# Optimization experiments

Hardware: AMD Instinct MI355X
Metric: run time of the kernel (lower is better)

The kernel has to match this reference:

```python
import jax, jax.numpy as jnp
import numpy as np
from jax import lax

B_, H_, W_ = 2, 32, 32
D_MODEL, D_STATE, D_CONV, DT_RANK, K = 192, 16, 3, 12, 4
D_INNER = 2 * D_MODEL


def setup_inputs() -> dict:
    key = jax.random.key(0)
    ks = jax.random.split(key, 10)
    x = jax.random.normal(ks[0], (B_, H_, W_, D_MODEL), jnp.float32)
    x_cross = jax.random.normal(ks[1], (B_, H_, W_, D_MODEL), jnp.float32)
    in_proj_w = jax.random.normal(ks[2], (2 * D_INNER, D_MODEL), jnp.float32) * 0.02
    in_proj_cross_w = jax.random.normal(ks[3], (D_INNER, D_MODEL), jnp.float32) * 0.02
    conv_w = jax.random.normal(ks[4], (D_INNER, 1, D_CONV, D_CONV), jnp.float32) * 0.1  # depthwise
    conv_b = jnp.zeros((D_INNER,), jnp.float32)
    x_proj_weight = jax.random.normal(ks[5], (K, DT_RANK + 2 * D_STATE, D_INNER), jnp.float32) * 0.02
    dt_std = DT_RANK ** -0.5
    dt_projs_weight = jax.random.uniform(ks[6], (K, D_INNER, DT_RANK), jnp.float32, -dt_std, dt_std)
    # inverse-softplus init of dt bias, as in CSS2D.dt_init
    dt = jnp.exp(jax.random.uniform(ks[7], (K, D_INNER), jnp.float32)
                 * (np.log(0.1) - np.log(0.001)) + np.log(0.001))
    dt = jnp.clip(dt, 1e-4, None)
    dt_projs_bias = dt + jnp.log(-jnp.expm1(-dt))
    A_logs = jnp.log(jnp.tile(jnp.arange(1, D_STATE + 1, dtype=jnp.float32)[None, :], (K * D_INNER, 1)))
    Ds = jnp.ones((K * D_INNER,), jnp.float32)
    out_norm_g = jnp.ones((D_INNER,), jnp.float32)
    out_norm_b = jnp.zeros((D_INNER,), jnp.float32)
    out_proj_w = jax.random.normal(ks[8], (D_MODEL, D_INNER), jnp.float32) * 0.02
    return dict(x=x, x_cross=x_cross, in_proj_w=in_proj_w, in_proj_cross_w=in_proj_cross_w,
                conv_w=conv_w, conv_b=conv_b, x_proj_weight=x_proj_weight,
                dt_projs_weight=dt_projs_weight, dt_projs_bias=dt_projs_bias,
                A_logs=A_logs, Ds=Ds, out_norm_g=out_norm_g, out_norm_b=out_norm_b,
                out_proj_w=out_proj_w)


def _css2d_forward(x, x_cross, in_proj_w, in_proj_cross_w, conv_w, conv_b,
                   x_proj_weight, dt_projs_weight, dt_projs_bias, A_logs, Ds,
                   out_norm_g, out_norm_b, out_proj_w):
    B, H, W, _ = x.shape
    L = H * W
    Din, N, R = D_INNER, D_STATE, DT_RANK

    # in projections
    xz = x @ in_proj_w.T                       # [B,H,W,2*Din]
    xp, z = jnp.split(xz, 2, axis=-1)
    xc = x_cross @ in_proj_cross_w.T           # [B,H,W,Din]

    # depthwise conv + SiLU on main branch (NCHW)
    xh = jnp.transpose(xp, (0, 3, 1, 2))
    pad = (D_CONV - 1) // 2
    xh = lax.conv_general_dilated(xh, conv_w, (1, 1), [(pad, pad), (pad, pad)],
                                  dimension_numbers=('NCHW', 'OIHW', 'NCHW'),
                                  feature_group_count=Din)
    xh = jax.nn.silu(xh + conv_b[None, :, None, None])
    xc = jnp.transpose(xc, (0, 3, 1, 2))       # [B,Din,H,W]

    def cross_scan(t):  # [B,Din,H,W] -> [B,4,Din,L]
        a = t.reshape(B, Din, L)
        b = jnp.transpose(t, (0, 1, 3, 2)).reshape(B, Din, L)
        s = jnp.stack([a, b], axis=1)
        return jnp.concatenate([s, jnp.flip(s, axis=-1)], axis=1)

    xs = cross_scan(xh)
    xsc = cross_scan(xc)

    # dt/B/C projections from the cross stream
    x_dbl = jnp.einsum('bkdl,kcd->bkcl', xsc, x_proj_weight)
    dts, Bmat, Cmat = jnp.split(x_dbl, [R, R + N], axis=2)  # [B,K,R,L],[B,K,N,L],[B,K,N,L]
    dts = jnp.einsum('bkrl,kdr->bkdl', dts, dt_projs_weight)

    A = -jnp.exp(A_logs).reshape(K, Din, N)
    delta = jax.nn.softplus(dts + dt_projs_bias[None, :, :, None])  # [B,K,Din,L]

    # selective scan: h_{t} = exp(delta*A)*h_{t-1} + delta*B_t*u_t ; y_t = C_t . h_t
    dA = jnp.exp(jnp.einsum('bkdl,kdn->lbkdn', delta, A))   # [L,B,K,Din,N]
    dBu = jnp.einsum('bkdl,bknl->lbkdn', delta * xs, Bmat)  # [L,B,K,Din,N]
    Ct = jnp.transpose(Cmat, (3, 0, 1, 2))                  # [L,B,K,N]

    def step(h, inp):
        dA_t, dBu_t, c = inp
        h = dA_t * h + dBu_t
        return h, jnp.einsum('bkdn,bkn->bkd', h, c)

    h0 = jnp.zeros((B, K, Din, N), x.dtype)
    _, ys = lax.scan(step, h0, (dA, dBu, Ct))               # ys: [L,B,K,Din]
    out_y = jnp.transpose(ys, (1, 2, 3, 0)) + xs * Ds.reshape(1, K, Din, 1)  # [B,K,Din,L]

    # merge the 4 directions
    inv_y = jnp.flip(out_y[:, 2:4], axis=-1)
    wh = lambda t: jnp.transpose(t.reshape(B, Din, W, H), (0, 1, 3, 2)).reshape(B, Din, L)
    y = out_y[:, 0] + inv_y[:, 0] + wh(out_y[:, 1]) + wh(inv_y[:, 1])
    y = jnp.transpose(y, (0, 2, 1)).reshape(B, H, W, Din)

    # LayerNorm(out_norm)
    mu = jnp.mean(y, axis=-1, keepdims=True)
    var = jnp.mean((y - mu) ** 2, axis=-1, keepdims=True)
    y = (y - mu) * lax.rsqrt(var + 1e-5) * out_norm_g + out_norm_b

    y = y * jax.nn.silu(z)
    return y @ out_proj_w.T


def reference(x, x_cross, in_proj_w, in_proj_cross_w, conv_w, conv_b, x_proj_weight,
              dt_projs_weight, dt_projs_bias, A_logs, Ds, out_norm_g, out_norm_b, out_proj_w):
    return _css2d_forward(x, x_cross, in_proj_w, in_proj_cross_w, conv_w, conv_b,
                          x_proj_weight, dt_projs_weight, dt_projs_bias, A_logs, Ds,
                          out_norm_g, out_norm_b, out_proj_w)
```

## Files before the change

### kernel.cpp

```cpp
#include <hip/hip_runtime.h>
#include <hip/hip_bf16.h>
#include <math.h>

#define BB 2
#define HH 32
#define WW 32
#define LL 1024
#define DM 192
#define DI 384
#define NS 16
#define RR 12
#define KK 4
#define CC 44
#define NC 64
#define LC 16
#define NCH 3072
#define GB 49152

__device__ __forceinline__ int bfflag(const void* dsv){
  return ((const unsigned*)dsv)[0] != 0x3F800000u;
}
__device__ __forceinline__ float ldin(const void* p, int i, int bf) {
  if (bf) {
    unsigned v = ((const unsigned short*)p)[i];
    return __uint_as_float(v << 16);
  }
  return ((const float*)p)[i];
}
__device__ __forceinline__ float4 ldin4(const void* p, int i, int bf) {
  if (bf) {
    ushort4 u = ((const ushort4*)p)[i >> 2];
    float4 r;
    r.x = __uint_as_float((unsigned)u.x << 16);
    r.y = __uint_as_float((unsigned)u.y << 16);
    r.z = __uint_as_float((unsigned)u.z << 16);
    r.w = __uint_as_float((unsigned)u.w << 16);
    return r;
  }
  return ((const float4*)p)[i >> 2];
}
__device__ __forceinline__ float sigm(float x){ return 1.f/(1.f + __expf(-x)); }
__device__ __forceinline__ float softplusf(float x){ return (x > 20.f) ? x : log1pf(__expf(x)); }

__device__ __forceinline__ int permk(int k, int l){
  if (k == 0) return l;
  if (k == 2) return LL-1-l;
  int lr = (k == 3) ? (LL-1-l) : l;
  return (lr & 31)*WW + (lr >> 5);
}

__global__ __launch_bounds__(256) void k_inproj(const void* x, const void* xcr,
    const void* wi, const void* wc, const void* dsv,
    float* __restrict__ xp, float* __restrict__ z, float* __restrict__ xcd){
  const int bf = bfflag(dsv);
  __shared__ float As[64][65];
  __shared__ float Ws[64][65];
  const int mb = blockIdx.x & 31;
  const int nb = blockIdx.x >> 5;
  const int pos0 = mb*64;
  const int row0g = nb*64;
  const void* src  = (row0g < 768) ? x  : xcr;
  const void* wsrc = (row0g < 768) ? wi : wc;
  const int wrow0 = (row0g < 768) ? row0g : row0g - 768;
  const int t = threadIdx.x;
  const int tx = t & 15, ty = t >> 4;
  float acc[4][4];
  #pragma unroll
  for (int m=0;m<4;m++){
    #pragma unroll
    for (int n=0;n<4;n++) acc[m][n]=0.f;
  }
  for (int k0 = 0; k0 < DM; k0 += 64){
    for (int i = t*4; i < 4096; i += 1024){
      const int p = i >> 6, kk = i & 63;
      const float4 va = ldin4(src,  (pos0 +p)*DM + k0 + kk, bf);
      As[kk+0][p]=va.x; As[kk+1][p]=va.y; As[kk+2][p]=va.z; As[kk+3][p]=va.w;
      const float4 vw = ldin4(wsrc, (wrow0+p)*DM + k0 + kk, bf);
      Ws[kk+0][p]=vw.x; Ws[kk+1][p]=vw.y; Ws[kk+2][p]=vw.z; Ws[kk+3][p]=vw.w;
    }
    __syncthreads();
    #pragma unroll 8
    for (int kk = 0; kk < 64; kk++){
      const float4 a4 = *(const float4*)&As[kk][ty*4];
      const float4 w4 = *(const float4*)&Ws[kk][tx*4];
      acc[0][0]=fmaf(a4.x,w4.x,acc[0][0]); acc[0][1]=fmaf(a4.x,w4.y,acc[0][1]);
      acc[0][2]=fmaf(a4.x,w4.z,acc[0][2]); acc[0][3]=fmaf(a4.x,w4.w,acc[0][3]);
      acc[1][0]=fmaf(a4.y,w4.x,acc[1][0]); acc[1][1]=fmaf(a4.y,w4.y,acc[1][1]);
      acc[1][2]=fmaf(a4.y,w4.z,acc[1][2]); acc[1][3]=fmaf(a4.y,w4.w,acc[1][3]);
      acc[2][0]=fmaf(a4.z,w4.x,acc[2][0]); acc[2][1]=fmaf(a4.z,w4.y,acc[2][1]);
      acc[2][2]=fmaf(a4.z,w4.z,acc[2][2]); acc[2][3]=fmaf(a4.z,w4.w,acc[2][3]);
      acc[3][0]=fmaf(a4.w,w4.x,acc[3][0]); acc[3][1]=fmaf(a4.w,w4.y,acc[3][1]);
      acc[3][2]=fmaf(a4.w,w4.z,acc[3][2]); acc[3][3]=fmaf(a4.w,w4.w,acc[3][3]);
    }
    __syncthreads();
  }
  float* dst; int obase;
  if (row0g < 384)      { dst = xp;  obase = row0g; }
  else if (row0g < 768) { dst = z;   obase = row0g-384; }
  else                  { dst = xcd; obase = row0g-768; }
  #pragma unroll
  for (int m=0;m<4;m++){
    const int pos = pos0 + ty*4 + m;
    *(float4*)&dst[(size_t)pos*DI + obase + tx*4] =
        make_float4(acc[m][0], acc[m][1], acc[m][2], acc[m][3]);
  }
}

__global__ __launch_bounds__(256) void k_conv(const float* __restrict__ xp,
    const void* cw, const void* cb, const void* dsv, float* __restrict__ xh){
  const int bf = bfflag(dsv);
  const int idx = blockIdx.x*256 + threadIdx.x;
  const int d = idx % DI;
  const int l = (idx / DI) % LL;
  const int b = idx / (DI*LL);
  const int h = l >> 5, w = l & 31;
  float acc = ldin(cb, d, bf);
  #pragma unroll
  for (int kh=0; kh<3; kh++){
    const int hh = h + kh - 1;
    if (hh < 0 || hh >= HH) continue;
    #pragma unroll
    for (int kw=0; kw<3; kw++){
      const int ww2 = w + kw - 1;
      if (ww2 < 0 || ww2 >= WW) continue;
      acc = fmaf(xp[(b*LL + hh*WW + ww2)*DI + d], ldin(cw, d*9 + kh*3 + kw, bf), acc);
    }
  }
  xh[idx] = acc * sigm(acc);
}

__global__ __launch_bounds__(384) void k_xscanA(const float* __restrict__ xc,
    const float* __restrict__ xh, const void* xpw, const void* dtw,
    const void* dtb, const void* alogs, const void* dsv,
    float* __restrict__ delta, float* __restrict__ Bm, float* __restrict__ Cm,
    float* __restrict__ Acum, float* __restrict__ Hend){
  const int bf = bfflag(dsv);
  const int blk = blockIdx.x;
  const int b = blk >> 8;
  const int k = (blk >> 6) & 3;
  const int c = blk & 63;
  const int l0 = c * LC;
  const int t = threadIdx.x;
  __shared__ float xrow[LC][DI+4];
  __shared__ float dtsS[LC][RR];
  __shared__ float Bs[LC][NS];
  for (int idx = t; idx < LC*96; idx += 384){
    const int j = idx / 96, cc = idx % 96;
    const int pl = permk(k, l0 + j);
    *(float4*)&xrow[j][cc*4] = *(const float4*)&xc[(b*LL + pl)*DI + cc*4];
  }
  __syncthreads();
  for (int idx = t; idx < CC*LC; idx += 384){
    const int ch = idx >> 4, j = idx & 15;
    const int wbase = (k*CC + ch)*DI;
    float a0=0.f, a1=0.f, a2=0.f, a3=0.f;
    for (int cc = 0; cc < 96; cc += 4){
      const float4 w0 = ldin4(xpw, wbase + (cc+0)*4, bf);
      const float4 w1 = ldin4(xpw, wbase + (cc+1)*4, bf);
      const float4 w2 = ldin4(xpw, wbase + (cc+2)*4, bf);
      const float4 w3 = ldin4(xpw, wbase + (cc+3)*4, bf);
      const float4 x0 = *(const float4*)&xrow[j][(cc+0)*4];
      const float4 x1 = *(const float4*)&xrow[j][(cc+1)*4];
      const float4 x2 = *(const float4*)&xrow[j][(cc+2)*4];
      const float4 x3 = *(const float4*)&xrow[j][(cc+3)*4];
      a0 = fmaf(w0.x,x0.x, fmaf(w0.y,x0.y, fmaf(w0.z,x0.z, fmaf(w0.w,x0.w, a0))));
      a1 = fmaf(w1.x,x1.x, fmaf(w1.y,x1.y, fmaf(w1.z,x1.z, fmaf(w1.w,x1.w, a1))));
      a2 = fmaf(w2.x,x2.x, fmaf(w2.y,x2.y, fmaf(w2.z,x2.z, fmaf(w2.w,x2.w, a2))));
      a3 = fmaf(w3.x,x3.x, fmaf(w3.y,x3.y, fmaf(w3.z,x3.z, fmaf(w3.w,x3.w, a3))));
    }
    const float acc = (a0+a1)+(a2+a3);
    if (ch < RR)          dtsS[j][ch] = acc;
    else if (ch < RR+NS){ Bs[j][ch-RR] = acc;
                          Bm[((b*KK+k)*LL + l0+j)*NS + (ch-RR)]    = acc; }
    else                  Cm[((b*KK+k)*LL + l0+j)*NS + (ch-RR-NS)] = acc;
  }
  __syncthreads();
  {
    const int d = t;
    float w[RR];
    #pragma unroll
    for (int q = 0; q < 3; q++){
      const float4 w4 = ldin4(dtw, (k*DI+d)*RR + q*4, bf);
      w[q*4+0]=w4.x; w[q*4+1]=w4.y; w[q*4+2]=w4.z; w[q*4+3]=w4.w;
    }
    const float bias = ldin(dtb, k*DI + d, bf);
    #pragma unroll
    for (int j = 0; j < LC; j++){
      float acc = bias;
      #pragma unroll
      for (int r = 0; r < RR; r++) acc = fmaf(w[r], dtsS[j][r], acc);
      xrow[j][d] = softplusf(acc);
    }
  }
  __syncthreads();
  for (int idx = t; idx < LC*96; idx += 384){
    const int j = idx / 96, cc = idx % 96;
    *(float4*)&delta[((b*KK+k)*LL + l0+j)*DI + cc*4] = *(const float4*)&xrow[j][cc*4];
  }
  {
    const int d = t;
    float An[NS];
    #pragma unroll
    for (int q = 0; q < 4; q++){
      const float4 a4 = ldin4(alogs, (k*DI + d)*NS + q*4, bf);
      An[q*4+0] = -__expf(a4.x); An[q*4+1] = -__expf(a4.y);
      An[q*4+2] = -__expf(a4.z); An[q*4+3] = -__expf(a4.w);
    }
    float h[NS], Ac[NS];
    #pragma unroll
    for (int n = 0; n < NS; n++){ h[n] = 0.f; Ac[n] = 1.f; }
    const int xbase = b*LL*DI + d;
    #pragma unroll 4
    for (int j = 0; j < LC; j++){
      const int l = l0 + j;
      const float dl = xrow[j][d];
      const float u  = xh[xbase + permk(k,l)*DI];
      const float dlu = dl*u;
      #pragma unroll
      for (int n = 0; n < NS; n++){
        const float e = __expf(dl*An[n]);
        Ac[n] *= e;
        h[n] = fmaf(e, h[n], dlu*Bs[j][n]);
      }
    }
    const int chain = (b*KK + k)*DI + d;
    const int obase = (c*NCH + chain)*NS;
    #pragma unroll
    for (int q = 0; q < 4; q++){
      *(float4*)&Acum[obase + q*4] = make_float4(Ac[q*4],Ac[q*4+1],Ac[q*4+2],Ac[q*4+3]);
      *(float4*)&Hend[obase + q*4] = make_float4(h[q*4],h[q*4+1],h[q*4+2],h[q*4+3]);
    }
  }
}

__global__ __launch_bounds__(256) void k_scanB(const float* __restrict__ Acum,
    float* __restrict__ Hend){
  const int g = blockIdx.x*256 + threadIdx.x;
  float h = 0.f;
  #pragma unroll 8
  for (int c = 0; c < NC; c++){
    const float a = Acum[c*GB + g];
    const float e = Hend[c*GB + g];
    Hend[c*GB + g] = h;
    h = fmaf(a, h, e);
  }
}

__global__ __launch_bounds__(256) void k_scanC(const float* __restrict__ delta,
    const float* __restrict__ xh, const float* __restrict__ Bm,
    const float* __restrict__ Cm, const void* alogs, const void* dsv,
    const float* __restrict__ Hin, float* __restrict__ ybuf){
  const int bf = bfflag(dsv);
  const int c = blockIdx.x / 12;
  const int chain = (blockIdx.x % 12)*256 + threadIdx.x;
  const int d = chain % DI;
  const int k = (chain / DI) & 3;
  const int b = chain / (DI*KK);
  float An[NS];
  #pragma unroll
  for (int q = 0; q < 4; q++){
    const float4 a4 = ldin4(alogs, (k*DI + d)*NS + q*4, bf);
    An[q*4+0] = -__expf(a4.x); An[q*4+1] = -__expf(a4.y);
    An[q*4+2] = -__expf(a4.z); An[q*4+3] = -__expf(a4.w);
  }
  float h[NS];
  const int ibase = (c*NCH + chain)*NS;
  #pragma unroll
  for (int q = 0; q < 4; q++){
    const float4 h4 = *(const float4*)&Hin[ibase + q*4];
    h[q*4+0]=h4.x; h[q*4+1]=h4.y; h[q*4+2]=h4.z; h[q*4+3]=h4.w;
  }
  const int lb = (b*KK+k)*LL;
  const int xbase = b*LL*DI + d;
  const int l0 = c*LC;
  #pragma unroll 4
  for (int l = l0; l < l0+LC; l++){
    const float dl = delta[(lb + l)*DI + d];
    const float u  = xh[xbase + permk(k,l)*DI];
    const float dlu = dl*u;
    const float4 B0 = *(const float4*)&Bm[(lb+l)*NS + 0];
    const float4 B1 = *(const float4*)&Bm[(lb+l)*NS + 4];
    const float4 B2 = *(const float4*)&Bm[(lb+l)*NS + 8];
    const float4 B3 = *(const float4*)&Bm[(lb+l)*NS + 12];
    const float4 C0 = *(const float4*)&Cm[(lb+l)*NS + 0];
    const float4 C1 = *(const float4*)&Cm[(lb+l)*NS + 4];
    const float4 C2 = *(const float4*)&Cm[(lb+l)*NS + 8];
    const float4 C3 = *(const float4*)&Cm[(lb+l)*NS + 12];
    const float Bv[NS] = {B0.x,B0.y,B0.z,B0.w, B1.x,B1.y,B1.z,B1.w,
                          B2.x,B2.y,B2.z,B2.w, B3.x,B3.y,B3.z,B3.w};
    const float Cv[NS] = {C0.x,C0.y,C0.z,C0.w, C1.x,C1.y,C1.z,C1.w,
                          C2.x,C2.y,C2.z,C2.w, C3.x,C3.y,C3.z,C3.w};
    float y = 0.f;
    #pragma unroll
    for (int n = 0; n < NS; n++){
      const float e = __expf(dl*An[n]);
      h[n] = fmaf(e, h[n], dlu*Bv[n]);
      y = fmaf(h[n], Cv[n], y);
    }
    ybuf[(lb + l)*DI + d] = y;
  }
}

__global__ __launch_bounds__(256) void k_merge(const float* __restrict__ scanY,
    const float* __restrict__ xh, const float* __restrict__ z,
    const void* dsP, const void* gP, const void* bP, const void* woP,
    void* out){
  const int bf = bfflag(dsP);
  const int blk = blockIdx.x;
  const int t = threadIdx.x;
  const int wv = t >> 6, lane = t & 63;
  __shared__ float ygs[4][DI];
  {
    const int j = wv;
    const int pos = blk*4 + j;
    const int b = pos >> 10, l = pos & 1023;
    const int lt = (l & 31)*32 + (l >> 5);
    float yv[6];
    float s = 0.f, s2 = 0.f;
    #pragma unroll
    for (int i = 0; i < 6; i++){
      const int d = i*64 + lane;
      float y = scanY[((b*KK+0)*LL + l        )*DI + d]
              + scanY[((b*KK+2)*LL + (LL-1-l ))*DI + d]
              + scanY[((b*KK+1)*LL + lt       )*DI + d]
              + scanY[((b*KK+3)*LL + (LL-1-lt))*DI + d];
      const float dsum = ldin(dsP, d, bf) + ldin(dsP, DI+d, bf)
                       + ldin(dsP, 2*DI+d, bf) + ldin(dsP, 3*DI+d, bf);
      y = fmaf(xh[(b*LL+l)*DI + d], dsum, y);
      yv[i] = y;
      s += y; s2 = fmaf(y, y, s2);
    }
    #pragma unroll
    for (int m = 1; m < 64; m <<= 1){
      s  += __shfl_xor(s,  m);
      s2 += __shfl_xor(s2, m);
    }
    const float mu = s * (1.f/DI);
    const float var = fmaxf(s2 * (1.f/DI) - mu*mu, 0.f);
    const float rs = rsqrtf(var + 1e-5f);
    #pragma unroll
    for (int i = 0; i < 6; i++){
      const int d = i*64 + lane;
      const float yn = (yv[i]-mu)*rs*ldin(gP, d, bf) + ldin(bP, d, bf);
      const float zg = z[(b*LL+l)*DI + d];
      ygs[j][d] = yn * zg * sigm(zg);
    }
  }
  __syncthreads();
  if (t < DM){
    const int o = t;
    float acc[4];
    #pragma unroll
    for (int j=0;j<4;j++) acc[j] = 0.f;
    for (int cc = 0; cc < 96; cc++){
      const float4 w4 = ldin4(woP, o*DI + cc*4, bf);
      #pragma unroll
      for (int j=0;j<4;j++){
        const float4 y4 = *(const float4*)&ygs[j][cc*4];
        acc[j] = fmaf(w4.x, y4.x, acc[j]);
        acc[j] = fmaf(w4.y, y4.y, acc[j]);
        acc[j] = fmaf(w4.z, y4.z, acc[j]);
        acc[j] = fmaf(w4.w, y4.w, acc[j]);
      }
    }
    #pragma unroll
    for (int j=0;j<4;j++){
      const int pos = blk*4 + j;
      if (bf) ((__hip_bfloat16*)out)[pos*DM + o] = __float2bfloat16(acc[j]);
      else    ((float*)out)[pos*DM + o] = acc[j];
    }
  }
}

extern "C" void kernel_launch(void* const* d_in, const int* in_sizes, int n_in,
                              void* d_out, int out_size, void* d_ws, size_t ws_size,
                              hipStream_t stream){
  const void* x    = d_in[0];
  const void* xcr  = d_in[1];
  const void* wi   = d_in[2];
  const void* wc   = d_in[3];
  const void* cw   = d_in[4];
  const void* cb   = d_in[5];
  const void* xpw  = d_in[6];
  const void* dtw  = d_in[7];
  const void* dtb  = d_in[8];
  const void* alog = d_in[9];
  const void* dsv  = d_in[10];
  const void* gno  = d_in[11];
  const void* bno  = d_in[12];
  const void* wo   = d_in[13];

  float* ws = (float*)d_ws;
  float* xp    = ws + 16;
  float* z     = xp    + (size_t)BB*LL*DI;
  float* xc    = z     + (size_t)BB*LL*DI;
  float* xh    = xc    + (size_t)BB*LL*DI;
  float* delta = xh    + (size_t)BB*LL*DI;
  float* Bm    = delta + (size_t)BB*KK*LL*DI;
  float* Cm    = Bm    + (size_t)BB*KK*LL*NS;
  float* Acum  = Cm    + (size_t)BB*KK*LL*NS;
  float* Hend  = Acum  + (size_t)GB*NC;
  float* ybuf  = Hend  + (size_t)GB*NC;

  k_inproj<<<18*32, 256, 0, stream>>>(x, xcr, wi, wc, dsv, xp, z, xc);
  k_conv  <<<BB*LL*DI/256, 256, 0, stream>>>(xp, cw, cb, dsv, xh);
  k_xscanA<<<BB*KK*NC, 384, 0, stream>>>(xc, xh, xpw, dtw, dtb, alog, dsv,
                                         delta, Bm, Cm, Acum, Hend);
  k_scanB <<<GB/256, 256, 0, stream>>>(Acum, Hend);
  k_scanC <<<NCH*NC/256, 256, 0, stream>>>(delta, xh, Bm, Cm, alog, dsv, Hend, ybuf);
  k_merge <<<BB*LL/4, 256, 0, stream>>>(ybuf, xh, z, dsv, gno, bno, wo, d_out);
}
```

Before: 223.9 us.

## Recompute delta in scanC from low-rank dts instead of storing full delta

Instead of writing the full delta tensor (B*K*L*DI floats) from k_xscanA and reading it back in k_scanC, only the 12-wide dt-rank projections are stored, and k_scanC recomputes softplus(W*dts+b) per channel. k_scanC is also restructured to one block per (b,k,chunk) with B/C/dts staged in shared memory instead of per-thread vector loads. This trades a large global write+read for a small amount of extra FMA and softplus work, and removes a barrier plus the staged delta store in xscanA.

```diff
diff --git a/kernel.cpp b/kernel.cpp
--- a/kernel.cpp
+++ b/kernel.cpp
@@ -132,7 +132,7 @@
 __global__ __launch_bounds__(384) void k_xscanA(const float* __restrict__ xc,
     const float* __restrict__ xh, const void* xpw, const void* dtw,
     const void* dtb, const void* alogs, const void* dsv,
-    float* __restrict__ delta, float* __restrict__ Bm, float* __restrict__ Cm,
+    float* __restrict__ dtsG, float* __restrict__ Bm, float* __restrict__ Cm,
     float* __restrict__ Acum, float* __restrict__ Hend){
   const int bf = bfflag(dsv);
   const int blk = blockIdx.x;
@@ -144,6 +144,7 @@
   __shared__ float xrow[LC][DI+4];
   __shared__ float dtsS[LC][RR];
   __shared__ float Bs[LC][NS];
+  const int lb = (b*KK+k)*LL;
   for (int idx = t; idx < LC*96; idx += 384){
     const int j = idx / 96, cc = idx % 96;
     const int pl = permk(k, l0 + j);
@@ -169,10 +170,11 @@
       a3 = fmaf(w3.x,x3.x, fmaf(w3.y,x3.y, fmaf(w3.z,x3.z, fmaf(w3.w,x3.w, a3))));
     }
     const float acc = (a0+a1)+(a2+a3);
-    if (ch < RR)          dtsS[j][ch] = acc;
+    if (ch < RR){         dtsS[j][ch] = acc;
+                          dtsG[(lb + l0+j)*RR + ch] = acc; }
     else if (ch < RR+NS){ Bs[j][ch-RR] = acc;
-                          Bm[((b*KK+k)*LL + l0+j)*NS + (ch-RR)]    = acc; }
-    else                  Cm[((b*KK+k)*LL + l0+j)*NS + (ch-RR-NS)] = acc;
+                          Bm[(lb + l0+j)*NS + (ch-RR)]    = acc; }
+    else                  Cm[(lb + l0+j)*NS + (ch-RR-NS)] = acc;
   }
   __syncthreads();
   {
@@ -184,21 +186,14 @@
       w[q*4+0]=w4.x; w[q*4+1]=w4.y; w[q*4+2]=w4.z; w[q*4+3]=w4.w;
     }
     const float bias = ldin(dtb, k*DI + d, bf);
+    float dl[LC];
     #pragma unroll
     for (int j = 0; j < LC; j++){
       float acc = bias;
       #pragma unroll
       for (int r = 0; r < RR; r++) acc = fmaf(w[r], dtsS[j][r], acc);
-      xrow[j][d] = softplusf(acc);
-    }
-  }
-  __syncthreads();
-  for (int idx = t; idx < LC*96; idx += 384){
-    const int j = idx / 96, cc = idx % 96;
-    *(float4*)&delta[((b*KK+k)*LL + l0+j)*DI + cc*4] = *(const float4*)&xrow[j][cc*4];
-  }
-  {
-    const int d = t;
+      dl[j] = softplusf(acc);
+    }
     float An[NS];
     #pragma unroll
     for (int q = 0; q < 4; q++){
@@ -212,13 +207,12 @@
     const int xbase = b*LL*DI + d;
     #pragma unroll 4
     for (int j = 0; j < LC; j++){
-      const int l = l0 + j;
-      const float dl = xrow[j][d];
-      const float u  = xh[xbase + permk(k,l)*DI];
-      const float dlu = dl*u;
+      const float dlj = dl[j];
+      const float u  = xh[xbase + permk(k, l0+j)*DI];
+      const float dlu = dlj*u;
       #pragma unroll
       for (int n = 0; n < NS; n++){
-        const float e = __expf(dl*An[n]);
+        const float e = __expf(dlj*An[n]);
         Ac[n] *= e;
         h[n] = fmaf(e, h[n], dlu*Bs[j][n]);
       }
@@ -246,16 +240,45 @@
   }
 }
 
-__global__ __launch_bounds__(256) void k_scanC(const float* __restrict__ delta,
-    const float* __restrict__ xh, const float* __restrict__ Bm,
-    const float* __restrict__ Cm, const void* alogs, const void* dsv,
+__global__ __launch_bounds__(384) void k_scanC(const float* __restrict__ xh,
+    const float* __restrict__ dtsG, const float* __restrict__ Bm,
+    const float* __restrict__ Cm, const void* dtw, const void* dtb,
+    const void* alogs, const void* dsv,
     const float* __restrict__ Hin, float* __restrict__ ybuf){
   const int bf = bfflag(dsv);
-  const int c = blockIdx.x / 12;
-  const int chain = (blockIdx.x % 12)*256 + threadIdx.x;
-  const int d = chain % DI;
-  const int k = (chain / DI) & 3;
-  const int b = chain / (DI*KK);
+  const int blk = blockIdx.x;
+  const int b = blk >> 8;
+  const int k = (blk >> 6) & 3;
+  const int c = blk & 63;
+  const int l0 = c * LC;
+  const int t = threadIdx.x;
+  __shared__ float dtsS[LC][RR];
+  __shared__ float Bs[LC][NS];
+  __shared__ float Cs[LC][NS];
+  const int lb = (b*KK+k)*LL;
+  for (int idx = t; idx < CC*LC; idx += 384){
+    const int ch = idx >> 4, j = idx & 15;
+    if (ch < RR)         dtsS[j][ch]      = dtsG[(lb + l0+j)*RR + ch];
+    else if (ch < RR+NS) Bs[j][ch-RR]     = Bm[(lb + l0+j)*NS + (ch-RR)];
+    else                 Cs[j][ch-RR-NS]  = Cm[(lb + l0+j)*NS + (ch-RR-NS)];
+  }
+  __syncthreads();
+  const int d = t;
+  float w[RR];
+  #pragma unroll
+  for (int q = 0; q < 3; q++){
+    const float4 w4 = ldin4(dtw, (k*DI+d)*RR + q*4, bf);
+    w[q*4+0]=w4.x; w[q*4+1]=w4.y; w[q*4+2]=w4.z; w[q*4+3]=w4.w;
+  }
+  const float bias = ldin(dtb, k*DI + d, bf);
+  float dl[LC];
+  #pragma unroll
+  for (int j = 0; j < LC; j++){
+    float acc = bias;
+    #pragma unroll
+    for (int r = 0; r < RR; r++) acc = fmaf(w[r], dtsS[j][r], acc);
+    dl[j] = softplusf(acc);
+  }
   float An[NS];
   #pragma unroll
   for (int q = 0; q < 4; q++){
@@ -264,40 +287,27 @@
     An[q*4+2] = -__expf(a4.z); An[q*4+3] = -__expf(a4.w);
   }
   float h[NS];
+  const int chain = (b*KK + k)*DI + d;
   const int ibase = (c*NCH + chain)*NS;
   #pragma unroll
   for (int q = 0; q < 4; q++){
     const float4 h4 = *(const float4*)&Hin[ibase + q*4];
     h[q*4+0]=h4.x; h[q*4+1]=h4.y; h[q*4+2]=h4.z; h[q*4+3]=h4.w;
   }
-  const int lb = (b*KK+k)*LL;
   const int xbase = b*LL*DI + d;
-  const int l0 = c*LC;
   #pragma unroll 4
-  for (int l = l0; l < l0+LC; l++){
-    const float dl = delta[(lb + l)*DI + d];
-    const float u  = xh[xbase + permk(k,l)*DI];
-    const float dlu = dl*u;
-    const float4 B0 = *(const float4*)&Bm[(lb+l)*NS + 0];
-    const float4 B1 = *(const float4*)&Bm[(lb+l)*NS + 4];
-    const float4 B2 = *(const float4*)&Bm[(lb+l)*NS + 8];
-    const float4 B3 = *(const float4*)&Bm[(lb+l)*NS + 12];
-    const float4 C0 = *(const float4*)&Cm[(lb+l)*NS + 0];
-    const float4 C1 = *(const float4*)&Cm[(lb+l)*NS + 4];
-    const float4 C2 = *(const float4*)&Cm[(lb+l)*NS + 8];
-    const float4 C3 = *(const float4*)&Cm[(lb+l)*NS + 12];
-    const float Bv[NS] = {B0.x,B0.y,B0.z,B0.w, B1.x,B1.y,B1.z,B1.w,
-                          B2.x,B2.y,B2.z,B2.w, B3.x,B3.y,B3.z,B3.w};
-    const float Cv[NS] = {C0.x,C0.y,C0.z,C0.w, C1.x,C1.y,C1.z,C1.w,
-                          C2.x,C2.y,C2.z,C2.w, C3.x,C3.y,C3.z,C3.w};
+  for (int j = 0; j < LC; j++){
+    const float dlj = dl[j];
+    const float u  = xh[xbase + permk(k, l0+j)*DI];
+    const float dlu = dlj*u;
     float y = 0.f;
     #pragma unroll
     for (int n = 0; n < NS; n++){
-      const float e = __expf(dl*An[n]);
-      h[n] = fmaf(e, h[n], dlu*Bv[n]);
-      y = fmaf(h[n], Cv[n], y);
-    }
-    ybuf[(lb + l)*DI + d] = y;
+      const float e = __expf(dlj*An[n]);
+      h[n] = fmaf(e, h[n], dlu*Bs[j][n]);
+      y = fmaf(h[n], Cs[j][n], y);
+    }
+    ybuf[(lb + l0 + j)*DI + d] = y;
   }
 }
 
@@ -395,8 +405,8 @@
   float* z     = xp    + (size_t)BB*LL*DI;
   float* xc    = z     + (size_t)BB*LL*DI;
   float* xh    = xc    + (size_t)BB*LL*DI;
-  float* delta = xh    + (size_t)BB*LL*DI;
-  float* Bm    = delta + (size_t)BB*KK*LL*DI;
+  float* dts   = xh    + (size_t)BB*LL*DI;
+  float* Bm    = dts   + (size_t)BB*KK*LL*RR;
   float* Cm    = Bm    + (size_t)BB*KK*LL*NS;
   float* Acum  = Cm    + (size_t)BB*KK*LL*NS;
   float* Hend  = Acum  + (size_t)GB*NC;
@@ -405,8 +415,9 @@
   k_inproj<<<18*32, 256, 0, stream>>>(x, xcr, wi, wc, dsv, xp, z, xc);
   k_conv  <<<BB*LL*DI/256, 256, 0, stream>>>(xp, cw, cb, dsv, xh);
   k_xscanA<<<BB*KK*NC, 384, 0, stream>>>(xc, xh, xpw, dtw, dtb, alog, dsv,
-                                         delta, Bm, Cm, Acum, Hend);
+                                         dts, Bm, Cm, Acum, Hend);
   k_scanB <<<GB/256, 256, 0, stream>>>(Acum, Hend);
-  k_scanC <<<NCH*NC/256, 256, 0, stream>>>(delta, xh, Bm, Cm, alog, dsv, Hend, ybuf);
+  k_scanC <<<BB*KK*NC, 384, 0, stream>>>(xh, dts, Bm, Cm, dtw, dtb, alog, dsv,
+                                         Hend, ybuf);
   k_merge <<<BB*LL/4, 256, 0, stream>>>(ybuf, xh, z, dsv, gno, bno, wo, d_out);
 }
```

New measurement: 236.1 us. 5.5% more time.
